# Kernel tuning notes

Measured on AMD Instinct MI355X. Metric: run time of the kernel, lower is better.

Reference implementation:

```python
import jax, jax.numpy as jnp
import numpy as np

B, H, O, T = 256, 1024, 512, 128


def setup_inputs() -> dict:
    key = jax.random.key(0)
    ks = jax.random.split(key, 7)
    s = 1.0 / np.sqrt(H)
    return {
        "C": jax.random.normal(ks[0], (B, H), jnp.float32),
        "W_ih": jax.random.normal(ks[1], (4 * H, H), jnp.float32) * s,
        "W_hh": jax.random.normal(ks[2], (4 * H, H), jnp.float32) * s,
        "b_ih": jax.random.normal(ks[3], (4 * H,), jnp.float32) * s,
        "b_hh": jax.random.normal(ks[4], (4 * H,), jnp.float32) * s,
        "W_lin": jax.random.normal(ks[5], (O, H), jnp.float32) * s,
        "b_lin": jax.random.normal(ks[6], (O,), jnp.float32) * s,
        "max_seq_len": T,
    }


def reference(C, W_ih, W_hh, b_ih, b_hh, W_lin, b_lin, max_seq_len):
    batch, hid = C.shape
    # Input is the same C at every timestep -> precompute input projection once.
    x_proj = C @ W_ih.T + b_ih + b_hh  # [B, 4H]

    def step(carry, _):
        h, c = carry
        gates = x_proj + h @ W_hh.T  # [B, 4H]
        i, f, g, o = jnp.split(gates, 4, axis=-1)  # torch gate order i,f,g,o
        i = jax.nn.sigmoid(i)
        f = jax.nn.sigmoid(f)
        g = jnp.tanh(g)
        o = jax.nn.sigmoid(o)
        c = f * c + i * g
        h = o * jnp.tanh(c)
        y = h @ W_lin.T + b_lin  # [B, O]
        return (h, c), y

    h0 = jnp.zeros((batch, hid), C.dtype)
    c0 = jnp.zeros((batch, hid), C.dtype)
    _, ys = jax.lax.scan(step, (h0, c0), None, length=max_seq_len)
    return ys  # [T, B, O]
```

## Files before the change

### kernel.cpp

```cpp
#include <hip/hip_runtime.h>

typedef _Float16 f16;
typedef _Float16 f16x4 __attribute__((ext_vector_type(4)));
typedef _Float16 f16x8 __attribute__((ext_vector_type(8)));
typedef float f32x2 __attribute__((ext_vector_type(2)));
typedef float f32x4 __attribute__((ext_vector_type(4)));

#define LSTM_B 256
#define LSTM_H 1024
#define LSTM_O 512
#define LSTM_T 128
#define GATES 4096


__global__ void cvt4_kernel(const float4* __restrict__ src, f16x4* __restrict__ dst, int n4) {
  int i = blockIdx.x * blockDim.x + threadIdx.x;
  int st = gridDim.x * blockDim.x;
  for (; i < n4; i += st) {
    float4 v = src[i];
    f16x4 o; o[0] = (f16)v.x; o[1] = (f16)v.y; o[2] = (f16)v.z; o[3] = (f16)v.w;
    dst[i] = o;
  }
}

__global__ void pack_whh_kernel(const float* __restrict__ Whh, f16* __restrict__ Wpack) {
  int idx = blockIdx.x * 256 + threadIdx.x;
  int lane = idx & 63;
  int f = (idx >> 6) & 127;
  int hj = idx >> 13;
  int kc = f >> 3, s = (f >> 2) & 1, wn = (f >> 1) & 1, nt = f & 1;
  int c = wn * 32 + nt * 16 + (lane & 15);
  int row = (c >> 4) * 1024 + hj * 16 + (c & 15);
  int k0 = kc * 64 + s * 32 + (lane >> 4) * 8;
  const float* src = Whh + (size_t)row * LSTM_H + k0;
  float4 v0 = *(const float4*)src;
  float4 v1 = *(const float4*)(src + 4);
  f16x8 o;
  o[0] = (f16)v0.x; o[1] = (f16)v0.y; o[2] = (f16)v0.z; o[3] = (f16)v0.w;
  o[4] = (f16)v1.x; o[5] = (f16)v1.y; o[6] = (f16)v1.z; o[7] = (f16)v1.w;
  *(f16x8*)(Wpack + (size_t)idx * 8) = o;
}

__global__ __launch_bounds__(256) void gemm_bt_kernel(
    const f16* __restrict__ A, const f16* __restrict__ Bw,
    const float* __restrict__ bias0, const float* __restrict__ bias1,
    float* __restrict__ out, int M, int N, int K, int gn, int xswz, int blkA)
{
  __shared__ __align__(16) f16 As[64][72];
  __shared__ __align__(16) f16 Bs[64][72];
  int bx = blockIdx.x;
  if (xswz) { int n = gridDim.x; bx = (bx & 7) * (n >> 3) + (bx >> 3); }
  int mb = bx / gn;
  int m0 = mb * 64;
  int n0 = (bx - mb * gn) * 64;
  int tid = threadIdx.x;
  int lane = tid & 63, w = tid >> 6;
  int wm = w >> 1, wn = w & 1;
  int sr = tid >> 2, sseg = tid & 3;
  const f16* ga;
  size_t kadv;
  if (blkA) {
    int m = m0 + sr;
    ga = A + ((size_t)(m >> 8) * 256 + (size_t)sseg * 4 + ((m >> 6) & 3)) * 1024 + (m & 63) * 16;
    kadv = 16384;
  } else {
    ga = A + (size_t)(m0 + sr) * K + sseg * 16;
    kadv = 64;
  }
  const f16* gb = Bw + (size_t)(n0 + sr) * K + sseg * 16;
  f32x4 acc00 = {}, acc01 = {}, acc10 = {}, acc11 = {};
  f16x8 ra0 = *(const f16x8*)ga, ra1 = *(const f16x8*)(ga + 8);
  f16x8 rb0 = *(const f16x8*)gb, rb1 = *(const f16x8*)(gb + 8);
  for (int kc = 0; kc < K; kc += 64) {
    __syncthreads();
    *(f16x8*)&As[sr][sseg * 16]     = ra0;
    *(f16x8*)&As[sr][sseg * 16 + 8] = ra1;
    *(f16x8*)&Bs[sr][sseg * 16]     = rb0;
    *(f16x8*)&Bs[sr][sseg * 16 + 8] = rb1;
    __syncthreads();
    if (kc + 64 < K) {
      ga += kadv; gb += 64;
      ra0 = *(const f16x8*)ga; ra1 = *(const f16x8*)(ga + 8);
      rb0 = *(const f16x8*)gb; rb1 = *(const f16x8*)(gb + 8);
    }
    int g = lane >> 4, r = lane & 15;
    #pragma unroll
    for (int s = 0; s < 2; s++) {
      f16x8 a0 = *(const f16x8*)&As[wm * 32      + r][s * 32 + g * 8];
      f16x8 a1 = *(const f16x8*)&As[wm * 32 + 16 + r][s * 32 + g * 8];
      f16x8 b0 = *(const f16x8*)&Bs[wn * 32      + r][s * 32 + g * 8];
      f16x8 b1 = *(const f16x8*)&Bs[wn * 32 + 16 + r][s * 32 + g * 8];
      acc00 = __builtin_amdgcn_mfma_f32_16x16x32_f16(a0, b0, acc00, 0, 0, 0);
      acc01 = __builtin_amdgcn_mfma_f32_16x16x32_f16(a0, b1, acc01, 0, 0, 0);
      acc10 = __builtin_amdgcn_mfma_f32_16x16x32_f16(a1, b0, acc10, 0, 0, 0);
      acc11 = __builtin_amdgcn_mfma_f32_16x16x32_f16(a1, b1, acc11, 0, 0, 0);
    }
  }
  int gq = lane >> 4, rr = lane & 15;
  f32x4 accs[2][2] = {{acc00, acc01}, {acc10, acc11}};
  #pragma unroll
  for (int mt = 0; mt < 2; mt++)
    #pragma unroll
    for (int nt = 0; nt < 2; nt++) {
      int row = m0 + wm * 32 + mt * 16 + gq * 4;
      int col = n0 + wn * 32 + nt * 16 + rr;
      float bv = bias0 ? bias0[col] : 0.f;
      if (bias1) bv += bias1[col];
      #pragma unroll
      for (int j = 0; j < 4; j++)
        out[(size_t)(row + j) * N + col] = accs[mt][nt][j] + bv;
    }
}

__device__ __forceinline__ void wait_chunk(const unsigned* p) {
  while (__hip_atomic_load(p, __ATOMIC_RELAXED, __HIP_MEMORY_SCOPE_AGENT) < 4u)
    __builtin_amdgcn_s_sleep(2);
  asm volatile("" ::: "memory");
}

__global__ __launch_bounds__(256, 1) void lstm_persist_kernel(
    const f16* __restrict__ Wpack, const float* __restrict__ xp,
    f16* __restrict__ hist, unsigned* __restrict__ ready)
{
  __shared__ __align__(16) f16 Bres[65536];
  __shared__ float gsm[64][65];

  const int wg = blockIdx.x;
  const int mb = (wg & 7) >> 1;
  const int hj = ((wg >> 3) << 1) | (wg & 1);
  const int m0 = mb * 64;
  const int tid = threadIdx.x;
  const int lane = tid & 63, w = tid >> 6;
  const int wm = w >> 1, wn = w & 1;
  const int g = lane >> 4, r = lane & 15;

  {
    const f16x8* src = (const f16x8*)(Wpack + (size_t)hj * 65536);
    f16x8* dst = (f16x8*)Bres;
    for (int i = tid; i < 8192; i += 256) dst[i] = src[i];
  }

  const int b_loc = tid & 63, hh0 = tid >> 6;
  const float* xprow = xp + (size_t)(m0 + b_loc) * GATES + hj * 16 + hh0 * 4;
  float4 xi = *(const float4*)(xprow);
  float4 xf = *(const float4*)(xprow + LSTM_H);
  float4 xg = *(const float4*)(xprow + 2 * LSTM_H);
  float4 xo = *(const float4*)(xprow + 3 * LSTM_H);
  float xiv[4] = {xi.x, xi.y, xi.z, xi.w};
  float xfv[4] = {xf.x, xf.y, xf.z, xf.w};
  float xgv[4] = {xg.x, xg.y, xg.z, xg.w};
  float xov[4] = {xo.x, xo.y, xo.z, xo.w};
  float cvv[4] = {0.f, 0.f, 0.f, 0.f};

  const int inv = (g >> 1) * 4096 + mb * 1024 + wm * 512 + r * 16 + (g & 1) * 8;
  const int stag = hj >> 2;
  const int bbo = wn * 2048 + lane * 16;
  f16* hob = hist + ((size_t)hj * 4 + mb) * 1024 + b_loc * 16 + hh0 * 4;
  unsigned* myflag = ready + (size_t)mb * 256 + (size_t)(hj >> 2) * 16;

  __syncthreads();

  for (int t = 0; t < LSTM_T; t++) {
    f32x4 acc00 = {}, acc01 = {}, acc10 = {}, acc11 = {};
    if (t > 0) {
      const f16* hb = hist + (size_t)(t - 1) * 262144 + inv;
      const unsigned* rdt = ready + (size_t)(t - 1) * 1024 + (size_t)mb * 256;
      f16x8 sA[3][4];
      #pragma unroll
      for (int j = 0; j < 3; j++) {
        const int kc = (stag + j) & 15;
        wait_chunk(rdt + kc * 16);
        const f16* p = hb + kc * 16384;
        sA[j][0] = *(const f16x8*)(p);
        sA[j][1] = *(const f16x8*)(p + 256);
        sA[j][2] = *(const f16x8*)(p + 8192);
        sA[j][3] = *(const f16x8*)(p + 8448);
      }
      #pragma unroll
      for (int i = 0; i < 16; i++) {
        const int kc = (stag + i) & 15;
        const int st = i % 3;
        const char* Bb = (const char*)Bres + kc * 8192;
        f16x8 b00 = *(const f16x8*)(Bb + bbo);
        f16x8 b10 = *(const f16x8*)(Bb + bbo + 1024);
        f16x8 b01 = *(const f16x8*)(Bb + 4096 + bbo);
        f16x8 b11 = *(const f16x8*)(Bb + 4096 + bbo + 1024);
        acc00 = __builtin_amdgcn_mfma_f32_16x16x32_f16(sA[st][0], b00, acc00, 0, 0, 0);
        acc01 = __builtin_amdgcn_mfma_f32_16x16x32_f16(sA[st][0], b10, acc01, 0, 0, 0);
        acc10 = __builtin_amdgcn_mfma_f32_16x16x32_f16(sA[st][1], b00, acc10, 0, 0, 0);
        acc11 = __builtin_amdgcn_mfma_f32_16x16x32_f16(sA[st][1], b10, acc11, 0, 0, 0);
        acc00 = __builtin_amdgcn_mfma_f32_16x16x32_f16(sA[st][2], b01, acc00, 0, 0, 0);
        acc01 = __builtin_amdgcn_mfma_f32_16x16x32_f16(sA[st][2], b11, acc01, 0, 0, 0);
        acc10 = __builtin_amdgcn_mfma_f32_16x16x32_f16(sA[st][3], b01, acc10, 0, 0, 0);
        acc11 = __builtin_amdgcn_mfma_f32_16x16x32_f16(sA[st][3], b11, acc11, 0, 0, 0);
        if (i + 3 < 16) {
          const int kn = (stag + i + 3) & 15;
          wait_chunk(rdt + kn * 16);
          const f16* p = hb + kn * 16384;
          sA[st][0] = *(const f16x8*)(p);
          sA[st][1] = *(const f16x8*)(p + 256);
          sA[st][2] = *(const f16x8*)(p + 8192);
          sA[st][3] = *(const f16x8*)(p + 8448);
        }
      }
    }
    {
      f32x4 accs[2][2] = {{acc00, acc01}, {acc10, acc11}};
      #pragma unroll
      for (int mt = 0; mt < 2; mt++)
        #pragma unroll
        for (int nt = 0; nt < 2; nt++)
          #pragma unroll
          for (int j = 0; j < 4; j++)
            gsm[wm * 32 + mt * 16 + g * 4 + j][wn * 32 + nt * 16 + r] = accs[mt][nt][j];
    }
    __syncthreads();
    float hnew[4];
    #pragma unroll
    for (int u = 0; u < 4; u++) {
      int hh = hh0 * 4 + u;
      float iv = gsm[b_loc][hh]      + xiv[u];
      float fv = gsm[b_loc][16 + hh] + xfv[u];
      float gv = gsm[b_loc][32 + hh] + xgv[u];
      float ov = gsm[b_loc][48 + hh] + xov[u];
      iv = 1.f / (1.f + __expf(-iv));
      fv = 1.f / (1.f + __expf(-fv));
      gv = 2.f / (1.f + __expf(-2.f * gv)) - 1.f;
      ov = 1.f / (1.f + __expf(-ov));
      float cn = fv * cvv[u] + iv * gv;
      cvv[u] = cn;
      float tc = 2.f / (1.f + __expf(-2.f * cn)) - 1.f;
      hnew[u] = ov * tc;
    }
    f16x4 hw; hw[0] = (f16)hnew[0]; hw[1] = (f16)hnew[1]; hw[2] = (f16)hnew[2]; hw[3] = (f16)hnew[3];
    {
      union { f16x4 h; f32x2 f2; } hu; hu.h = hw;
      f16* haddr = hob + (size_t)t * 262144;
      asm volatile("global_store_dwordx2 %0, %1, off sc0 sc1" :: "v"(haddr), "v"(hu.f2) : "memory");
    }
    asm volatile("s_waitcnt vmcnt(0)" ::: "memory");
    __syncthreads();
    if (tid == 0)
      __hip_atomic_fetch_add(myflag + (size_t)t * 1024, 1u,
                             __ATOMIC_RELAXED, __HIP_MEMORY_SCOPE_AGENT);
  }
}

extern "C" void kernel_launch(void* const* d_in, const int* in_sizes, int n_in,
                              void* d_out, int out_size, void* d_ws, size_t ws_size,
                              hipStream_t stream)
{
  (void)in_sizes; (void)n_in; (void)out_size; (void)ws_size;
  const float* C     = (const float*)d_in[0];
  const float* W_ih  = (const float*)d_in[1];
  const float* W_hh  = (const float*)d_in[2];
  const float* b_ih  = (const float*)d_in[3];
  const float* b_hh  = (const float*)d_in[4];
  const float* W_lin = (const float*)d_in[5];
  const float* b_lin = (const float*)d_in[6];

  char* ws = (char*)d_ws;
  size_t off = 0;
  auto alloc = [&](size_t bytes) { void* p = ws + off; off += (bytes + 255) & ~(size_t)255; return p; };
  f16*      Wih16  = (f16*)alloc((size_t)GATES * LSTM_H * 2);
  f16*      Wlin16 = (f16*)alloc((size_t)LSTM_O * LSTM_H * 2);
  f16*      C16    = (f16*)alloc((size_t)LSTM_B * LSTM_H * 2);
  f16*      Wpack  = (f16*)alloc((size_t)GATES * LSTM_H * 2);
  float*    xp     = (float*)alloc((size_t)LSTM_B * GATES * 4);
  f16*      hist   = (f16*)alloc((size_t)LSTM_T * LSTM_B * LSTM_H * 2);
  unsigned* ready  = (unsigned*)alloc((size_t)LSTM_T * 1024 * 4);

  cvt4_kernel<<<2048, 256, 0, stream>>>((const float4*)W_ih,  (f16x4*)Wih16,  GATES * LSTM_H / 4);
  cvt4_kernel<<<512,  256, 0, stream>>>((const float4*)W_lin, (f16x4*)Wlin16, LSTM_O * LSTM_H / 4);
  cvt4_kernel<<<256,  256, 0, stream>>>((const float4*)C,     (f16x4*)C16,    LSTM_B * LSTM_H / 4);
  pack_whh_kernel<<<2048, 256, 0, stream>>>(W_hh, Wpack);
  hipMemsetAsync(ready, 0, (size_t)LSTM_T * 1024 * 4, stream);

  gemm_bt_kernel<<<(LSTM_B / 64) * (GATES / 64), 256, 0, stream>>>(
      C16, Wih16, b_ih, b_hh, xp, LSTM_B, GATES, LSTM_H, GATES / 64, 0, 0);

  {
    const f16* wp = Wpack; const float* xpp = xp; f16* hp = hist; unsigned* rp = ready;
    void* args[] = { (void*)&wp, (void*)&xpp, (void*)&hp, (void*)&rp };
    hipLaunchCooperativeKernel((void*)lstm_persist_kernel, dim3(256), dim3(256), args, 0, stream);
  }

  gemm_bt_kernel<<<(LSTM_T * LSTM_B / 64) * (LSTM_O / 64), 256, 0, stream>>>(
      hist, Wlin16, b_lin, nullptr, (float*)d_out,
      LSTM_T * LSTM_B, LSTM_O, LSTM_H, LSTM_O / 64, 1, 1);
}
```

Before: 930.5 us.

## Replace per-chunk readiness flags with a single per-batch-block counter and rewarp MFMA tiling

Each block now waits once per timestep on one counter per batch block, which all 64 producer blocks increment, instead of polling a separate flag before each of 16 K-chunks. The warp tiling changes from 2x2 (32x32 per warp) to 1x4 (16 rows by 64 columns per warp), so each warp loads half as many A fragments from global memory and more B fragments from LDS. The final step no longer signals. The single wait gives up the chunk-by-chunk overlap between arriving producers and compute, and the hb pointer adds f>>7, which is always zero, presumably to create a data dependency on the flag load.

Result: slower. 1.066 ms (+14.6%).

```diff
diff --git a/kernel.cpp b/kernel.cpp
--- a/kernel.cpp
+++ b/kernel.cpp
@@ -112,12 +112,6 @@
     }
 }
 
-__device__ __forceinline__ void wait_chunk(const unsigned* p) {
-  while (__hip_atomic_load(p, __ATOMIC_RELAXED, __HIP_MEMORY_SCOPE_AGENT) < 4u)
-    __builtin_amdgcn_s_sleep(2);
-  asm volatile("" ::: "memory");
-}
-
 __global__ __launch_bounds__(256, 1) void lstm_persist_kernel(
     const f16* __restrict__ Wpack, const float* __restrict__ xp,
     f16* __restrict__ hist, unsigned* __restrict__ ready)
@@ -131,7 +125,6 @@
   const int m0 = mb * 64;
   const int tid = threadIdx.x;
   const int lane = tid & 63, w = tid >> 6;
-  const int wm = w >> 1, wn = w & 1;
   const int g = lane >> 4, r = lane & 15;
 
   {
@@ -152,67 +145,66 @@
   float xov[4] = {xo.x, xo.y, xo.z, xo.w};
   float cvv[4] = {0.f, 0.f, 0.f, 0.f};
 
-  const int inv = (g >> 1) * 4096 + mb * 1024 + wm * 512 + r * 16 + (g & 1) * 8;
+  const int ainv = (g >> 1) * 4096 + mb * 1024 + w * 256 + r * 16 + (g & 1) * 8;
   const int stag = hj >> 2;
-  const int bbo = wn * 2048 + lane * 16;
+  const char* Bb0 = (const char*)Bres + lane * 16;
   f16* hob = hist + ((size_t)hj * 4 + mb) * 1024 + b_loc * 16 + hh0 * 4;
-  unsigned* myflag = ready + (size_t)mb * 256 + (size_t)(hj >> 2) * 16;
 
   __syncthreads();
 
   for (int t = 0; t < LSTM_T; t++) {
-    f32x4 acc00 = {}, acc01 = {}, acc10 = {}, acc11 = {};
+    f32x4 acc0 = {}, acc1 = {}, acc2 = {}, acc3 = {};
     if (t > 0) {
-      const f16* hb = hist + (size_t)(t - 1) * 262144 + inv;
-      const unsigned* rdt = ready + (size_t)(t - 1) * 1024 + (size_t)mb * 256;
-      f16x8 sA[3][4];
-      #pragma unroll
-      for (int j = 0; j < 3; j++) {
-        const int kc = (stag + j) & 15;
-        wait_chunk(rdt + kc * 16);
-        const f16* p = hb + kc * 16384;
-        sA[j][0] = *(const f16x8*)(p);
-        sA[j][1] = *(const f16x8*)(p + 256);
-        sA[j][2] = *(const f16x8*)(p + 8192);
-        sA[j][3] = *(const f16x8*)(p + 8448);
+      const unsigned* flagp = ready + ((size_t)(t - 1) * 4 + mb) * 16;
+      unsigned f;
+      for (;;) {
+        f = __hip_atomic_load(flagp, __ATOMIC_RELAXED, __HIP_MEMORY_SCOPE_AGENT);
+        if (f >= 64u) break;
+        __builtin_amdgcn_s_sleep(1);
+      }
+      const f16* hb = hist + (size_t)(t - 1) * 262144 + ainv + (f >> 7);
+      f16x8 sa0[4], sa1[4];
+      #pragma unroll
+      for (int i = 0; i < 3; i++) {
+        const int kc = (stag + i) & 15;
+        sa0[i] = *(const f16x8*)(hb + kc * 16384);
+        sa1[i] = *(const f16x8*)(hb + kc * 16384 + 8192);
       }
       #pragma unroll
       for (int i = 0; i < 16; i++) {
         const int kc = (stag + i) & 15;
-        const int st = i % 3;
-        const char* Bb = (const char*)Bres + kc * 8192;
-        f16x8 b00 = *(const f16x8*)(Bb + bbo);
-        f16x8 b10 = *(const f16x8*)(Bb + bbo + 1024);
-        f16x8 b01 = *(const f16x8*)(Bb + 4096 + bbo);
-        f16x8 b11 = *(const f16x8*)(Bb + 4096 + bbo + 1024);
-        acc00 = __builtin_amdgcn_mfma_f32_16x16x32_f16(sA[st][0], b00, acc00, 0, 0, 0);
-        acc01 = __builtin_amdgcn_mfma_f32_16x16x32_f16(sA[st][0], b10, acc01, 0, 0, 0);
-        acc10 = __builtin_amdgcn_mfma_f32_16x16x32_f16(sA[st][1], b00, acc10, 0, 0, 0);
-        acc11 = __builtin_amdgcn_mfma_f32_16x16x32_f16(sA[st][1], b10, acc11, 0, 0, 0);
-        acc00 = __builtin_amdgcn_mfma_f32_16x16x32_f16(sA[st][2], b01, acc00, 0, 0, 0);
-        acc01 = __builtin_amdgcn_mfma_f32_16x16x32_f16(sA[st][2], b11, acc01, 0, 0, 0);
-        acc10 = __builtin_amdgcn_mfma_f32_16x16x32_f16(sA[st][3], b01, acc10, 0, 0, 0);
-        acc11 = __builtin_amdgcn_mfma_f32_16x16x32_f16(sA[st][3], b11, acc11, 0, 0, 0);
         if (i + 3 < 16) {
           const int kn = (stag + i + 3) & 15;
-          wait_chunk(rdt + kn * 16);
-          const f16* p = hb + kn * 16384;
-          sA[st][0] = *(const f16x8*)(p);
-          sA[st][1] = *(const f16x8*)(p + 256);
-          sA[st][2] = *(const f16x8*)(p + 8192);
-          sA[st][3] = *(const f16x8*)(p + 8448);
+          sa0[(i + 3) & 3] = *(const f16x8*)(hb + kn * 16384);
+          sa1[(i + 3) & 3] = *(const f16x8*)(hb + kn * 16384 + 8192);
         }
+        const char* Bb = Bb0 + kc * 8192;
+        f16x8 b00 = *(const f16x8*)(Bb);
+        f16x8 b01 = *(const f16x8*)(Bb + 1024);
+        f16x8 b02 = *(const f16x8*)(Bb + 2048);
+        f16x8 b03 = *(const f16x8*)(Bb + 3072);
+        f16x8 b10 = *(const f16x8*)(Bb + 4096);
+        f16x8 b11 = *(const f16x8*)(Bb + 5120);
+        f16x8 b12 = *(const f16x8*)(Bb + 6144);
+        f16x8 b13 = *(const f16x8*)(Bb + 7168);
+        const f16x8 a0 = sa0[i & 3], a1 = sa1[i & 3];
+        acc0 = __builtin_amdgcn_mfma_f32_16x16x32_f16(a0, b00, acc0, 0, 0, 0);
+        acc1 = __builtin_amdgcn_mfma_f32_16x16x32_f16(a0, b01, acc1, 0, 0, 0);
+        acc2 = __builtin_amdgcn_mfma_f32_16x16x32_f16(a0, b02, acc2, 0, 0, 0);
+        acc3 = __builtin_amdgcn_mfma_f32_16x16x32_f16(a0, b03, acc3, 0, 0, 0);
+        acc0 = __builtin_amdgcn_mfma_f32_16x16x32_f16(a1, b10, acc0, 0, 0, 0);
+        acc1 = __builtin_amdgcn_mfma_f32_16x16x32_f16(a1, b11, acc1, 0, 0, 0);
+        acc2 = __builtin_amdgcn_mfma_f32_16x16x32_f16(a1, b12, acc2, 0, 0, 0);
+        acc3 = __builtin_amdgcn_mfma_f32_16x16x32_f16(a1, b13, acc3, 0, 0, 0);
       }
     }
     {
-      f32x4 accs[2][2] = {{acc00, acc01}, {acc10, acc11}};
-      #pragma unroll
-      for (int mt = 0; mt < 2; mt++)
+      f32x4 accs[4] = {acc0, acc1, acc2, acc3};
+      #pragma unroll
+      for (int n = 0; n < 4; n++)
         #pragma unroll
-        for (int nt = 0; nt < 2; nt++)
-          #pragma unroll
-          for (int j = 0; j < 4; j++)
-            gsm[wm * 32 + mt * 16 + g * 4 + j][wn * 32 + nt * 16 + r] = accs[mt][nt][j];
+        for (int j = 0; j < 4; j++)
+          gsm[w * 16 + g * 4 + j][n * 16 + r] = accs[n][j];
     }
     __syncthreads();
     float hnew[4];
@@ -238,11 +230,13 @@
       f16* haddr = hob + (size_t)t * 262144;
       asm volatile("global_store_dwordx2 %0, %1, off sc0 sc1" :: "v"(haddr), "v"(hu.f2) : "memory");
     }
-    asm volatile("s_waitcnt vmcnt(0)" ::: "memory");
-    __syncthreads();
-    if (tid == 0)
-      __hip_atomic_fetch_add(myflag + (size_t)t * 1024, 1u,
-                             __ATOMIC_RELAXED, __HIP_MEMORY_SCOPE_AGENT);
+    if (t + 1 < LSTM_T) {
+      asm volatile("s_waitcnt vmcnt(0)" ::: "memory");
+      __syncthreads();
+      if (tid == 0)
+        __hip_atomic_fetch_add(ready + ((size_t)t * 4 + mb) * 16, 1u,
+                               __ATOMIC_RELAXED, __HIP_MEMORY_SCOPE_AGENT);
+    }
   }
 }
 
@@ -268,13 +262,13 @@
   f16*      Wpack  = (f16*)alloc((size_t)GATES * LSTM_H * 2);
   float*    xp     = (float*)alloc((size_t)LSTM_B * GATES * 4);
   f16*      hist   = (f16*)alloc((size_t)LSTM_T * LSTM_B * LSTM_H * 2);
-  unsigned* ready  = (unsigned*)alloc((size_t)LSTM_T * 1024 * 4);
+  unsigned* ready  = (unsigned*)alloc((size_t)LSTM_T * 4 * 16 * 4);
 
   cvt4_kernel<<<2048, 256, 0, stream>>>((const float4*)W_ih,  (f16x4*)Wih16,  GATES * LSTM_H / 4);
   cvt4_kernel<<<512,  256, 0, stream>>>((const float4*)W_lin, (f16x4*)Wlin16, LSTM_O * LSTM_H / 4);
   cvt4_kernel<<<256,  256, 0, stream>>>((const float4*)C,     (f16x4*)C16,    LSTM_B * LSTM_H / 4);
   pack_whh_kernel<<<2048, 256, 0, stream>>>(W_hh, Wpack);
-  hipMemsetAsync(ready, 0, (size_t)LSTM_T * 1024 * 4, stream);
+  hipMemsetAsync(ready, 0, (size_t)LSTM_T * 4 * 16 * 4, stream);
 
   gemm_bt_kernel<<<(LSTM_B / 64) * (GATES / 64), 256, 0, stream>>>(
       C16, Wih16, b_ih, b_hh, xp, LSTM_B, GATES, LSTM_H, GATES / 64, 0, 0);
```

## Batch-prefetch readiness flags and deepen h-chunk pipeline to four slots

Applied to the files above, without the earlier changes.

All 16 readiness flags for the previous step are loaded up front, so polling only happens on chunks not yet ready, and the h-chunk loads now carry an address dependency on the flag value (f>>5, which is zero) to enforce ordering. The A-operand ring grows from three to four slots and the next load is issued before the MFMAs of the current chunk. The final timestep skips the wait, barrier and flag increment because no later step consumes it. Register pressure rises from the extra prefetch slot and flag array.

New measurement: 1.014 ms. +8.9%, slower.

```diff
diff --git a/kernel.cpp b/kernel.cpp
--- a/kernel.cpp
+++ b/kernel.cpp
@@ -112,12 +112,6 @@
     }
 }
 
-__device__ __forceinline__ void wait_chunk(const unsigned* p) {
-  while (__hip_atomic_load(p, __ATOMIC_RELAXED, __HIP_MEMORY_SCOPE_AGENT) < 4u)
-    __builtin_amdgcn_s_sleep(2);
-  asm volatile("" ::: "memory");
-}
-
 __global__ __launch_bounds__(256, 1) void lstm_persist_kernel(
     const f16* __restrict__ Wpack, const float* __restrict__ xp,
     f16* __restrict__ hist, unsigned* __restrict__ ready)
@@ -154,23 +148,31 @@
 
   const int inv = (g >> 1) * 4096 + mb * 1024 + wm * 512 + r * 16 + (g & 1) * 8;
   const int stag = hj >> 2;
-  const int bbo = wn * 2048 + lane * 16;
+  const int bb = wn * 2048 + lane * 16;
   f16* hob = hist + ((size_t)hj * 4 + mb) * 1024 + b_loc * 16 + hh0 * 4;
-  unsigned* myflag = ready + (size_t)mb * 256 + (size_t)(hj >> 2) * 16;
 
   __syncthreads();
 
   for (int t = 0; t < LSTM_T; t++) {
     f32x4 acc00 = {}, acc01 = {}, acc10 = {}, acc11 = {};
     if (t > 0) {
+      const unsigned* rdt = ready + (size_t)(t - 1) * 1024 + (size_t)mb * 256;
+      unsigned fv[16];
+      #pragma unroll
+      for (int j = 0; j < 16; j++)
+        fv[j] = __hip_atomic_load(rdt + ((stag + j) & 15) * 16,
+                                  __ATOMIC_RELAXED, __HIP_MEMORY_SCOPE_AGENT);
       const f16* hb = hist + (size_t)(t - 1) * 262144 + inv;
-      const unsigned* rdt = ready + (size_t)(t - 1) * 1024 + (size_t)mb * 256;
-      f16x8 sA[3][4];
+      f16x8 sA[4][4];
       #pragma unroll
       for (int j = 0; j < 3; j++) {
         const int kc = (stag + j) & 15;
-        wait_chunk(rdt + kc * 16);
-        const f16* p = hb + kc * 16384;
+        unsigned f = fv[j];
+        while (f < 4u) {
+          __builtin_amdgcn_s_sleep(1);
+          f = __hip_atomic_load(rdt + kc * 16, __ATOMIC_RELAXED, __HIP_MEMORY_SCOPE_AGENT);
+        }
+        const f16* p = hb + kc * 16384 + (f >> 5);
         sA[j][0] = *(const f16x8*)(p);
         sA[j][1] = *(const f16x8*)(p + 256);
         sA[j][2] = *(const f16x8*)(p + 8192);
@@ -178,30 +180,35 @@
       }
       #pragma unroll
       for (int i = 0; i < 16; i++) {
-        const int kc = (stag + i) & 15;
-        const int st = i % 3;
-        const char* Bb = (const char*)Bres + kc * 8192;
-        f16x8 b00 = *(const f16x8*)(Bb + bbo);
-        f16x8 b10 = *(const f16x8*)(Bb + bbo + 1024);
-        f16x8 b01 = *(const f16x8*)(Bb + 4096 + bbo);
-        f16x8 b11 = *(const f16x8*)(Bb + 4096 + bbo + 1024);
-        acc00 = __builtin_amdgcn_mfma_f32_16x16x32_f16(sA[st][0], b00, acc00, 0, 0, 0);
-        acc01 = __builtin_amdgcn_mfma_f32_16x16x32_f16(sA[st][0], b10, acc01, 0, 0, 0);
-        acc10 = __builtin_amdgcn_mfma_f32_16x16x32_f16(sA[st][1], b00, acc10, 0, 0, 0);
-        acc11 = __builtin_amdgcn_mfma_f32_16x16x32_f16(sA[st][1], b10, acc11, 0, 0, 0);
-        acc00 = __builtin_amdgcn_mfma_f32_16x16x32_f16(sA[st][2], b01, acc00, 0, 0, 0);
-        acc01 = __builtin_amdgcn_mfma_f32_16x16x32_f16(sA[st][2], b11, acc01, 0, 0, 0);
-        acc10 = __builtin_amdgcn_mfma_f32_16x16x32_f16(sA[st][3], b01, acc10, 0, 0, 0);
-        acc11 = __builtin_amdgcn_mfma_f32_16x16x32_f16(sA[st][3], b11, acc11, 0, 0, 0);
         if (i + 3 < 16) {
           const int kn = (stag + i + 3) & 15;
-          wait_chunk(rdt + kn * 16);
-          const f16* p = hb + kn * 16384;
-          sA[st][0] = *(const f16x8*)(p);
-          sA[st][1] = *(const f16x8*)(p + 256);
-          sA[st][2] = *(const f16x8*)(p + 8192);
-          sA[st][3] = *(const f16x8*)(p + 8448);
+          unsigned f = fv[i + 3];
+          while (f < 4u) {
+            __builtin_amdgcn_s_sleep(1);
+            f = __hip_atomic_load(rdt + kn * 16, __ATOMIC_RELAXED, __HIP_MEMORY_SCOPE_AGENT);
+          }
+          const f16* p = hb + kn * 16384 + (f >> 5);
+          sA[(i + 3) & 3][0] = *(const f16x8*)(p);
+          sA[(i + 3) & 3][1] = *(const f16x8*)(p + 256);
+          sA[(i + 3) & 3][2] = *(const f16x8*)(p + 8192);
+          sA[(i + 3) & 3][3] = *(const f16x8*)(p + 8448);
         }
+        const int kc = (stag + i) & 15;
+        const char* Bb = (const char*)Bres + kc * 8192;
+        f16x8 b00 = *(const f16x8*)(Bb + bb);
+        f16x8 b10 = *(const f16x8*)(Bb + bb + 1024);
+        f16x8 b01 = *(const f16x8*)(Bb + 4096 + bb);
+        f16x8 b11 = *(const f16x8*)(Bb + 4096 + bb + 1024);
+        const f16x8 a0 = sA[i & 3][0], a1 = sA[i & 3][1];
+        const f16x8 a2 = sA[i & 3][2], a3 = sA[i & 3][3];
+        acc00 = __builtin_amdgcn_mfma_f32_16x16x32_f16(a0, b00, acc00, 0, 0, 0);
+        acc01 = __builtin_amdgcn_mfma_f32_16x16x32_f16(a0, b10, acc01, 0, 0, 0);
+        acc10 = __builtin_amdgcn_mfma_f32_16x16x32_f16(a1, b00, acc10, 0, 0, 0);
+        acc11 = __builtin_amdgcn_mfma_f32_16x16x32_f16(a1, b10, acc11, 0, 0, 0);
+        acc00 = __builtin_amdgcn_mfma_f32_16x16x32_f16(a2, b01, acc00, 0, 0, 0);
+        acc01 = __builtin_amdgcn_mfma_f32_16x16x32_f16(a2, b11, acc01, 0, 0, 0);
+        acc10 = __builtin_amdgcn_mfma_f32_16x16x32_f16(a3, b01, acc10, 0, 0, 0);
+        acc11 = __builtin_amdgcn_mfma_f32_16x16x32_f16(a3, b11, acc11, 0, 0, 0);
       }
     }
     {
@@ -220,14 +227,14 @@
     for (int u = 0; u < 4; u++) {
       int hh = hh0 * 4 + u;
       float iv = gsm[b_loc][hh]      + xiv[u];
-      float fv = gsm[b_loc][16 + hh] + xfv[u];
+      float fv2 = gsm[b_loc][16 + hh] + xfv[u];
       float gv = gsm[b_loc][32 + hh] + xgv[u];
       float ov = gsm[b_loc][48 + hh] + xov[u];
       iv = 1.f / (1.f + __expf(-iv));
-      fv = 1.f / (1.f + __expf(-fv));
+      fv2 = 1.f / (1.f + __expf(-fv2));
       gv = 2.f / (1.f + __expf(-2.f * gv)) - 1.f;
       ov = 1.f / (1.f + __expf(-ov));
-      float cn = fv * cvv[u] + iv * gv;
+      float cn = fv2 * cvv[u] + iv * gv;
       cvv[u] = cn;
       float tc = 2.f / (1.f + __expf(-2.f * cn)) - 1.f;
       hnew[u] = ov * tc;
@@ -238,11 +245,13 @@
       f16* haddr = hob + (size_t)t * 262144;
       asm volatile("global_store_dwordx2 %0, %1, off sc0 sc1" :: "v"(haddr), "v"(hu.f2) : "memory");
     }
-    asm volatile("s_waitcnt vmcnt(0)" ::: "memory");
-    __syncthreads();
-    if (tid == 0)
-      __hip_atomic_fetch_add(myflag + (size_t)t * 1024, 1u,
-                             __ATOMIC_RELAXED, __HIP_MEMORY_SCOPE_AGENT);
+    if (t + 1 < LSTM_T) {
+      asm volatile("s_waitcnt vmcnt(0)" ::: "memory");
+      __syncthreads();
+      if (tid == 0)
+        __hip_atomic_fetch_add(ready + (size_t)t * 1024 + (size_t)mb * 256 + (size_t)(hj >> 2) * 16,
+                               1u, __ATOMIC_RELAXED, __HIP_MEMORY_SCOPE_AGENT);
+    }
   }
 }
 
```
